# Kernel optimization log

Hardware: AMD Instinct MI355X
Metric: run time of the kernel (lower is better)

## Reference

```python
import jax, jax.numpy as jnp
import numpy as np

N = 100000   # nodes
E = 1600000  # edges
I_DIM = 512
H_DIM = 64   # hardcoded in GCNEncoder
Z_DIM = 64


def gcn_conv(x, W, b, src, dst, n):
    """GCNConv: D^{-1/2}(A+I)D^{-1/2} X W + b, edge weights = 1."""
    xw = x @ W  # [n, out]
    ones = jnp.ones(src.shape[0], dtype=xw.dtype)
    deg = jax.ops.segment_sum(ones, dst, num_segments=n) + 1.0  # +1 for self-loop
    dinv = jax.lax.rsqrt(deg)
    norm = dinv[src] * dinv[dst]  # [E]
    agg = jax.ops.segment_sum(xw[src] * norm[:, None], dst, num_segments=n)
    agg = agg + xw * (dinv * dinv)[:, None]  # self-loop term, norm = 1/deg
    return agg + b


def setup_inputs() -> dict:
    key = jax.random.key(0)
    ks = jax.random.split(key, 9)
    x = jax.random.normal(ks[0], (N, I_DIM), dtype=jnp.float32)
    edge_index = jax.random.randint(ks[1], (2, E), 0, N, dtype=jnp.int64)
    # glorot-ish init for weights
    W1 = jax.random.normal(ks[2], (I_DIM, H_DIM), jnp.float32) * (1.0 / np.sqrt(I_DIM))
    b1 = jnp.zeros((H_DIM,), jnp.float32)
    W_mu = jax.random.normal(ks[3], (H_DIM, Z_DIM), jnp.float32) * (1.0 / np.sqrt(H_DIM))
    b_mu = jnp.zeros((Z_DIM,), jnp.float32)
    W_var = jax.random.normal(ks[4], (H_DIM, Z_DIM), jnp.float32) * (1.0 / np.sqrt(H_DIM))
    b_var = jnp.zeros((Z_DIM,), jnp.float32)
    eps = jax.random.normal(ks[5], (N, Z_DIM), jnp.float32)  # reparameterization noise
    return {"x": x, "edge_index": edge_index, "W1": W1, "b1": b1,
            "W_mu": W_mu, "b_mu": b_mu, "W_var": W_var, "b_var": b_var,
            "eps": eps}


def reference(x, edge_index, W1, b1, W_mu, b_mu, W_var, b_var, eps):
    n = x.shape[0]
    src, dst = edge_index[0], edge_index[1]
    # encoder (eval mode: dropout is identity)
    h = jax.nn.relu(gcn_conv(x, W1, b1, src, dst, n))
    z_mean = gcn_conv(h, W_mu, b_mu, src, dst, n)
    z_var = jax.nn.softplus(gcn_conv(h, W_var, b_var, src, dst, n))
    # Normal(z_mean, z_var).rsample()
    z = z_mean + z_var * eps
    return z_mean, z_var, z
```

## Files before the change

kernel.cpp:

```cpp
#include <hip/hip_runtime.h>
#include <hip/hip_bf16.h>
#include <math.h>

#define IDIM 512
#define HDIM 64

typedef __attribute__((ext_vector_type(8))) short short8;
typedef __attribute__((ext_vector_type(4))) float f32x4;
typedef unsigned short u16;
typedef unsigned int u32;

__device__ __forceinline__ float bflo(u32 u) { return __uint_as_float(u << 16); }
__device__ __forceinline__ float bfhi(u32 u) { return __uint_as_float(u & 0xffff0000u); }


__global__ __launch_bounds__(256) void k_deg(const int* __restrict__ dst,
                                             int* __restrict__ deg, int E) {
    int e = blockIdx.x * blockDim.x + threadIdx.x;
    if (e < E) atomicAdd(&deg[dst[e]], 1);
}

__global__ __launch_bounds__(256) void k_blocksum(const int* __restrict__ deg,
                                                  int* __restrict__ bsum, int n) {
    __shared__ int sd[256];
    int b = blockIdx.x, tid = threadIdx.x;
    int base = b * 1024 + tid * 4;
    int s = 0;
#pragma unroll
    for (int k = 0; k < 4; k++) {
        int idx = base + k;
        if (idx < n) s += deg[idx];
    }
    sd[tid] = s;
    __syncthreads();
    for (int off = 128; off > 0; off >>= 1) {
        if (tid < off) sd[tid] += sd[tid + off];
        __syncthreads();
    }
    if (tid == 0) bsum[b] = sd[0];
}

__global__ __launch_bounds__(128) void k_scanbsum(const int* __restrict__ bsum,
                                                  int* __restrict__ boff, int B,
                                                  int* __restrict__ rowptr, int n, int E) {
    __shared__ int s[128];
    int t = threadIdx.x;
    int v = (t < B) ? bsum[t] : 0;
    s[t] = v;
    __syncthreads();
    for (int off = 1; off < 128; off <<= 1) {
        int u = (t >= off) ? s[t - off] : 0;
        __syncthreads();
        s[t] += u;
        __syncthreads();
    }
    if (t < B) boff[t] = s[t] - v;
    if (t == 0) rowptr[n] = E;
}

__global__ __launch_bounds__(256) void k_rowptr(const int* __restrict__ deg,
                                                const int* __restrict__ boff,
                                                int* __restrict__ rowptr,
                                                int* __restrict__ cursor,
                                                float* __restrict__ dinv, int n) {
    __shared__ int sd[256];
    int b = blockIdx.x, tid = threadIdx.x;
    int base = b * 1024 + tid * 4;
    int d[4];
    int tt = 0;
#pragma unroll
    for (int k = 0; k < 4; k++) {
        d[k] = (base + k < n) ? deg[base + k] : 0;
        tt += d[k];
    }
    sd[tid] = tt;
    __syncthreads();
    for (int off = 1; off < 256; off <<= 1) {
        int v = 0;
        if (tid >= off) v = sd[tid - off];
        __syncthreads();
        sd[tid] += v;
        __syncthreads();
    }
    int run = boff[b] + sd[tid] - tt;
#pragma unroll
    for (int k = 0; k < 4; k++) {
        if (base + k < n) {
            rowptr[base + k] = run;
            cursor[base + k] = run;
            dinv[base + k] = rsqrtf((float)d[k] + 1.0f);
            run += d[k];
        }
    }
}

__global__ __launch_bounds__(256) void k_build(const int* __restrict__ src,
                                               const int* __restrict__ dst,
                                               int* __restrict__ cursor,
                                               int* __restrict__ srcs, int E) {
    int e = blockIdx.x * blockDim.x + threadIdx.x;
    if (e >= E) return;
    int p = atomicAdd(&cursor[dst[e]], 1);
    srcs[p] = src[e];
}

__global__ __launch_bounds__(256) void k_prepB(const float* __restrict__ W1,
                                               short* __restrict__ Btg) {
    int id = blockIdx.x * 256 + threadIdx.x;
    if (id >= IDIM * HDIM) return;
    int k = id >> 6, nn = id & 63;
    __hip_bfloat16 b = __float2bfloat16(W1[id]);
    Btg[nn * IDIM + k] = *(short*)&b;
}

__global__ __launch_bounds__(256) void k_prepW2(const float* __restrict__ Wmu,
                                                const float* __restrict__ Wvar,
                                                short* __restrict__ Whi,
                                                short* __restrict__ Wlo) {
    int id = blockIdx.x * 256 + threadIdx.x;
    if (id >= 128 * 64) return;
    int c = id >> 6;
    int k = id & 63;
    float wv = (c < 64) ? Wmu[k * 64 + c] : Wvar[k * 64 + (c - 64)];
    __hip_bfloat16 h = __float2bfloat16(wv);
    float hf = __bfloat162float(h);
    __hip_bfloat16 l = __float2bfloat16(wv - hf);
    Whi[c * 64 + k] = *(short*)&h;
    Wlo[c * 64 + k] = *(short*)&l;
}

#define GM 128
#define KC 128
#define APAD 8
__global__ __launch_bounds__(256) void k_gemm1(const float* __restrict__ x,
                                               const short* __restrict__ Btg,
                                               const float* __restrict__ dinv,
                                               u16* __restrict__ g1, int n) {
    __shared__ short As[GM][KC + APAD];
    __shared__ short Bs[HDIM][KC + APAD];
    int tid = threadIdx.x;
    int row0 = blockIdx.x * GM;
    int w = tid >> 6, lane = tid & 63;
    int m = lane & 15, kb = lane >> 4;

    f32x4 acc[2][4];
#pragma unroll
    for (int rb = 0; rb < 2; rb++)
#pragma unroll
        for (int nt = 0; nt < 4; nt++) acc[rb][nt] = (f32x4){0.f, 0.f, 0.f, 0.f};

    for (int kc = 0; kc < IDIM; kc += KC) {
        __syncthreads();
#pragma unroll
        for (int i = 0; i < 16; i++) {
            int idx = tid + i * 256;
            int r = idx >> 5;
            int c4 = idx & 31;
            int grow = row0 + r;
            float4 v = make_float4(0.f, 0.f, 0.f, 0.f);
            if (grow < n) v = *(const float4*)&x[(size_t)grow * IDIM + kc + c4 * 4];
            __hip_bfloat162 h0 = __float22bfloat162_rn(make_float2(v.x, v.y));
            __hip_bfloat162 h1 = __float22bfloat162_rn(make_float2(v.z, v.w));
            int2 p;
            p.x = *(int*)&h0;
            p.y = *(int*)&h1;
            *(int2*)&As[r][c4 * 4] = p;
        }
#pragma unroll
        for (int i = 0; i < 4; i++) {
            int idx = tid + i * 256;
            int r = idx >> 4;
            int u8 = idx & 15;
            float4 v = *(const float4*)&Btg[(size_t)r * IDIM + kc + u8 * 8];
            *(float4*)&Bs[r][u8 * 8] = v;
        }
        __syncthreads();
#pragma unroll
        for (int ks = 0; ks < KC; ks += 32) {
            short8 a0 = *(const short8*)&As[w * 32 + m][ks + kb * 8];
            short8 a1 = *(const short8*)&As[w * 32 + 16 + m][ks + kb * 8];
            short8 b0 = *(const short8*)&Bs[m][ks + kb * 8];
            short8 b1 = *(const short8*)&Bs[16 + m][ks + kb * 8];
            short8 b2 = *(const short8*)&Bs[32 + m][ks + kb * 8];
            short8 b3 = *(const short8*)&Bs[48 + m][ks + kb * 8];
            acc[0][0] = __builtin_amdgcn_mfma_f32_16x16x32_bf16(a0, b0, acc[0][0], 0, 0, 0);
            acc[0][1] = __builtin_amdgcn_mfma_f32_16x16x32_bf16(a0, b1, acc[0][1], 0, 0, 0);
            acc[0][2] = __builtin_amdgcn_mfma_f32_16x16x32_bf16(a0, b2, acc[0][2], 0, 0, 0);
            acc[0][3] = __builtin_amdgcn_mfma_f32_16x16x32_bf16(a0, b3, acc[0][3], 0, 0, 0);
            acc[1][0] = __builtin_amdgcn_mfma_f32_16x16x32_bf16(a1, b0, acc[1][0], 0, 0, 0);
            acc[1][1] = __builtin_amdgcn_mfma_f32_16x16x32_bf16(a1, b1, acc[1][1], 0, 0, 0);
            acc[1][2] = __builtin_amdgcn_mfma_f32_16x16x32_bf16(a1, b2, acc[1][2], 0, 0, 0);
            acc[1][3] = __builtin_amdgcn_mfma_f32_16x16x32_bf16(a1, b3, acc[1][3], 0, 0, 0);
        }
    }
#pragma unroll
    for (int rb = 0; rb < 2; rb++) {
        int rbase = row0 + w * 32 + rb * 16 + kb * 4;
#pragma unroll
        for (int reg = 0; reg < 4; reg++) {
            int grow = rbase + reg;
            if (grow < n) {
                float dv = dinv[grow];
#pragma unroll
                for (int nt = 0; nt < 4; nt++) {
                    __hip_bfloat16 b = __float2bfloat16(acc[rb][nt][reg] * dv);
                    g1[(size_t)grow * HDIM + nt * 16 + m] = *(u16*)&b;
                }
            }
        }
    }
}

__global__ __launch_bounds__(256) void k_gather1(const int* __restrict__ rowptr,
                                                 const int* __restrict__ srcs,
                                                 const float* __restrict__ dinv,
                                                 const u16* __restrict__ g1,
                                                 const float* __restrict__ b1,
                                                 u16* __restrict__ g2, int n) {
    int tid = threadIdx.x;
    int r = tid >> 6, lane = tid & 63;
    int grp = lane >> 3, q = lane & 7;
    int i = blockIdx.x * 4 + r;
    if (i >= n) return;
    int beg = rowptr[i], end = rowptr[i + 1];
    float a[8];
#pragma unroll
    for (int k = 0; k < 8; k++) a[k] = 0.f;
    int j = beg + grp;
    for (; j + 8 < end; j += 16) {
        int s0 = srcs[j];
        int s1 = srcs[j + 8];
        uint4 u0 = *(const uint4*)&g1[(size_t)s0 * HDIM + q * 8];
        uint4 u1 = *(const uint4*)&g1[(size_t)s1 * HDIM + q * 8];
        a[0] += bflo(u0.x) + bflo(u1.x); a[1] += bfhi(u0.x) + bfhi(u1.x);
        a[2] += bflo(u0.y) + bflo(u1.y); a[3] += bfhi(u0.y) + bfhi(u1.y);
        a[4] += bflo(u0.z) + bflo(u1.z); a[5] += bfhi(u0.z) + bfhi(u1.z);
        a[6] += bflo(u0.w) + bflo(u1.w); a[7] += bfhi(u0.w) + bfhi(u1.w);
    }
    if (j < end) {
        int s0 = srcs[j];
        uint4 u0 = *(const uint4*)&g1[(size_t)s0 * HDIM + q * 8];
        a[0] += bflo(u0.x); a[1] += bfhi(u0.x);
        a[2] += bflo(u0.y); a[3] += bfhi(u0.y);
        a[4] += bflo(u0.z); a[5] += bfhi(u0.z);
        a[6] += bflo(u0.w); a[7] += bfhi(u0.w);
    }
#pragma unroll
    for (int k = 0; k < 8; k++) {
        a[k] += __shfl_xor(a[k], 8);
        a[k] += __shfl_xor(a[k], 16);
        a[k] += __shfl_xor(a[k], 32);
    }
    if (grp == 0) {
        uint4 us = *(const uint4*)&g1[(size_t)i * HDIM + q * 8];
        float s0 = bflo(us.x), s1 = bfhi(us.x), s2 = bflo(us.y), s3 = bfhi(us.y);
        float s4 = bflo(us.z), s5 = bfhi(us.z), s6 = bflo(us.w), s7 = bfhi(us.w);
        float4 bv0 = *(const float4*)&b1[q * 8];
        float4 bv1 = *(const float4*)&b1[q * 8 + 4];
        float di = dinv[i];
        float o0 = fmaxf(di * (a[0] + s0) + bv0.x, 0.f) * di;
        float o1 = fmaxf(di * (a[1] + s1) + bv0.y, 0.f) * di;
        float o2 = fmaxf(di * (a[2] + s2) + bv0.z, 0.f) * di;
        float o3 = fmaxf(di * (a[3] + s3) + bv0.w, 0.f) * di;
        float o4 = fmaxf(di * (a[4] + s4) + bv1.x, 0.f) * di;
        float o5 = fmaxf(di * (a[5] + s5) + bv1.y, 0.f) * di;
        float o6 = fmaxf(di * (a[6] + s6) + bv1.z, 0.f) * di;
        float o7 = fmaxf(di * (a[7] + s7) + bv1.w, 0.f) * di;
        __hip_bfloat162 p0 = __float22bfloat162_rn(make_float2(o0, o1));
        __hip_bfloat162 p1 = __float22bfloat162_rn(make_float2(o2, o3));
        __hip_bfloat162 p2 = __float22bfloat162_rn(make_float2(o4, o5));
        __hip_bfloat162 p3 = __float22bfloat162_rn(make_float2(o6, o7));
        uint4 w;
        w.x = *(u32*)&p0; w.y = *(u32*)&p1; w.z = *(u32*)&p2; w.w = *(u32*)&p3;
        *(uint4*)&g2[(size_t)i * HDIM + q * 8] = w;
    }
}

__global__ __launch_bounds__(256) void k_gather2(const int* __restrict__ rowptr,
                                                 const int* __restrict__ srcs,
                                                 const float* __restrict__ dinv,
                                                 const u16* __restrict__ g2,
                                                 float* __restrict__ hagg, int n) {
    int tid = threadIdx.x;
    int r = tid >> 6, lane = tid & 63;
    int grp = lane >> 3, q = lane & 7;
    int i = blockIdx.x * 4 + r;
    if (i >= n) return;
    int beg = rowptr[i], end = rowptr[i + 1];
    float a[8];
#pragma unroll
    for (int k = 0; k < 8; k++) a[k] = 0.f;
    int j = beg + grp;
    for (; j + 8 < end; j += 16) {
        int s0 = srcs[j];
        int s1 = srcs[j + 8];
        uint4 u0 = *(const uint4*)&g2[(size_t)s0 * HDIM + q * 8];
        uint4 u1 = *(const uint4*)&g2[(size_t)s1 * HDIM + q * 8];
        a[0] += bflo(u0.x) + bflo(u1.x); a[1] += bfhi(u0.x) + bfhi(u1.x);
        a[2] += bflo(u0.y) + bflo(u1.y); a[3] += bfhi(u0.y) + bfhi(u1.y);
        a[4] += bflo(u0.z) + bflo(u1.z); a[5] += bfhi(u0.z) + bfhi(u1.z);
        a[6] += bflo(u0.w) + bflo(u1.w); a[7] += bfhi(u0.w) + bfhi(u1.w);
    }
    if (j < end) {
        int s0 = srcs[j];
        uint4 u0 = *(const uint4*)&g2[(size_t)s0 * HDIM + q * 8];
        a[0] += bflo(u0.x); a[1] += bfhi(u0.x);
        a[2] += bflo(u0.y); a[3] += bfhi(u0.y);
        a[4] += bflo(u0.z); a[5] += bfhi(u0.z);
        a[6] += bflo(u0.w); a[7] += bfhi(u0.w);
    }
#pragma unroll
    for (int k = 0; k < 8; k++) {
        a[k] += __shfl_xor(a[k], 8);
        a[k] += __shfl_xor(a[k], 16);
        a[k] += __shfl_xor(a[k], 32);
    }
    if (grp == 0) {
        uint4 us = *(const uint4*)&g2[(size_t)i * HDIM + q * 8];
        float di = dinv[i];
        float4 o0, o1;
        o0.x = di * (a[0] + bflo(us.x));
        o0.y = di * (a[1] + bfhi(us.x));
        o0.z = di * (a[2] + bflo(us.y));
        o0.w = di * (a[3] + bfhi(us.y));
        o1.x = di * (a[4] + bflo(us.z));
        o1.y = di * (a[5] + bfhi(us.z));
        o1.z = di * (a[6] + bflo(us.w));
        o1.w = di * (a[7] + bfhi(us.w));
        *(float4*)&hagg[(size_t)i * HDIM + q * 8] = o0;
        *(float4*)&hagg[(size_t)i * HDIM + q * 8 + 4] = o1;
    }
}

__global__ __launch_bounds__(256) void k_gemm2(const float* __restrict__ hagg,
                                               const short* __restrict__ Whi,
                                               const short* __restrict__ Wlo,
                                               const float* __restrict__ bmu,
                                               const float* __restrict__ bvar,
                                               const float* __restrict__ eps,
                                               float* __restrict__ out, int n) {
    int tid = threadIdx.x;
    int w = tid >> 6, lane = tid & 63;
    int m = lane & 15, kb = lane >> 4;
    int row0 = blockIdx.x * 128 + w * 32;

    short8 ah[2][2], al[2][2];
#pragma unroll
    for (int rb = 0; rb < 2; rb++) {
#pragma unroll
        for (int ks = 0; ks < 2; ks++) {
            int grow = row0 + rb * 16 + m;
            float v[8];
            if (grow < n) {
                const float* base = &hagg[(size_t)grow * HDIM + ks * 32 + kb * 8];
                float4 v0 = *(const float4*)base;
                float4 v1 = *(const float4*)(base + 4);
                v[0] = v0.x; v[1] = v0.y; v[2] = v0.z; v[3] = v0.w;
                v[4] = v1.x; v[5] = v1.y; v[6] = v1.z; v[7] = v1.w;
            } else {
#pragma unroll
                for (int jj = 0; jj < 8; jj++) v[jj] = 0.f;
            }
#pragma unroll
            for (int jj = 0; jj < 8; jj++) {
                __hip_bfloat16 h = __float2bfloat16(v[jj]);
                float hf = __bfloat162float(h);
                __hip_bfloat16 l = __float2bfloat16(v[jj] - hf);
                ah[rb][ks][jj] = *(short*)&h;
                al[rb][ks][jj] = *(short*)&l;
            }
        }
    }

    f32x4 acc[2][8];
#pragma unroll
    for (int rb = 0; rb < 2; rb++)
#pragma unroll
        for (int nt = 0; nt < 8; nt++) acc[rb][nt] = (f32x4){0.f, 0.f, 0.f, 0.f};

#pragma unroll
    for (int nt = 0; nt < 8; nt++) {
#pragma unroll
        for (int ks = 0; ks < 2; ks++) {
            const short* bbase = &Whi[(size_t)(nt * 16 + m) * HDIM + ks * 32 + kb * 8];
            const short* lbase = &Wlo[(size_t)(nt * 16 + m) * HDIM + ks * 32 + kb * 8];
            short8 bh = *(const short8*)bbase;
            short8 bl = *(const short8*)lbase;
#pragma unroll
            for (int rb = 0; rb < 2; rb++) {
                acc[rb][nt] = __builtin_amdgcn_mfma_f32_16x16x32_bf16(ah[rb][ks], bh, acc[rb][nt], 0, 0, 0);
                acc[rb][nt] = __builtin_amdgcn_mfma_f32_16x16x32_bf16(al[rb][ks], bh, acc[rb][nt], 0, 0, 0);
                acc[rb][nt] = __builtin_amdgcn_mfma_f32_16x16x32_bf16(ah[rb][ks], bl, acc[rb][nt], 0, 0, 0);
            }
        }
    }

    size_t nh = (size_t)n * HDIM;
#pragma unroll
    for (int rb = 0; rb < 2; rb++) {
#pragma unroll
        for (int nt = 0; nt < 4; nt++) {
            int c = nt * 16 + m;
            float bm = bmu[c], bv = bvar[c];
#pragma unroll
            for (int reg = 0; reg < 4; reg++) {
                int grow = row0 + rb * 16 + kb * 4 + reg;
                if (grow < n) {
                    float mu = acc[rb][nt][reg] + bm;
                    float va = acc[rb][nt + 4][reg] + bv;
                    float zv = fmaxf(va, 0.f) + log1pf(expf(-fabsf(va)));
                    size_t o = (size_t)grow * HDIM + c;
                    float z = mu + zv * eps[o];
                    out[o] = mu;
                    out[nh + o] = zv;
                    out[2 * nh + o] = z;
                }
            }
        }
    }
}

extern "C" void kernel_launch(void* const* d_in, const int* in_sizes, int n_in,
                              void* d_out, int out_size, void* d_ws, size_t ws_size,
                              hipStream_t stream) {
    const float* x    = (const float*)d_in[0];
    const int*   ei   = (const int*)d_in[1];
    const float* W1   = (const float*)d_in[2];
    const float* b1   = (const float*)d_in[3];
    const float* Wmu  = (const float*)d_in[4];
    const float* bmu  = (const float*)d_in[5];
    const float* Wvar = (const float*)d_in[6];
    const float* bvar = (const float*)d_in[7];
    const float* eps  = (const float*)d_in[8];
    float* out = (float*)d_out;

    int n = in_sizes[0] / IDIM;
    int E = in_sizes[1] / 2;
    const int* src = ei;
    const int* dst = ei + E;

    char* p = (char*)d_ws;
    u16* bufB   = (u16*)p;               p += (size_t)n * HDIM * 2;
    float* hagg = (float*)p;             p += (size_t)n * HDIM * 4;
    u16* bufA   = (u16*)hagg;
    int* srcs   = (int*)p;               p += (size_t)E * 4;
    short* Btg  = (short*)p;             p += (size_t)IDIM * HDIM * 2;
    short* W2hi = (short*)p;             p += (size_t)128 * HDIM * 2;
    short* W2lo = (short*)p;             p += (size_t)128 * HDIM * 2;
    int* rowptr = (int*)p;               p += (size_t)(n + 1) * 4;
    int* cursor = (int*)p;               p += (size_t)n * 4;
    float* dinv = (float*)p;             p += (size_t)n * 4;
    int* bsum   = (int*)p;               p += 128 * 4;
    int* boff   = (int*)p;               p += 128 * 4;

    int B = (n + 1023) / 1024;

    hipMemsetAsync(cursor, 0, (size_t)n * sizeof(int), stream);
    k_deg<<<(E + 255) / 256, 256, 0, stream>>>(dst, cursor, E);
    k_blocksum<<<B, 256, 0, stream>>>(cursor, bsum, n);
    k_scanbsum<<<1, 128, 0, stream>>>(bsum, boff, B, rowptr, n, E);
    k_rowptr<<<B, 256, 0, stream>>>(cursor, boff, rowptr, cursor, dinv, n);
    k_build<<<(E + 255) / 256, 256, 0, stream>>>(src, dst, cursor, srcs, E);

    k_prepB<<<(IDIM * HDIM + 255) / 256, 256, 0, stream>>>(W1, Btg);
    k_prepW2<<<(128 * HDIM + 255) / 256, 256, 0, stream>>>(Wmu, Wvar, W2hi, W2lo);

    k_gemm1<<<(n + GM - 1) / GM, 256, 0, stream>>>(x, Btg, dinv, bufA, n);
    k_gather1<<<(n + 3) / 4, 256, 0, stream>>>(rowptr, srcs, dinv, bufA, b1, bufB, n);

    k_gather2<<<(n + 3) / 4, 256, 0, stream>>>(rowptr, srcs, dinv, bufB, hagg, n);
    k_gemm2<<<(n + 127) / 128, 256, 0, stream>>>(hagg, W2hi, W2lo, bmu, bvar, eps, out, n);
}
```

Measured before the change: 714.7 us.

## Build CSR via two-level bucket partition with shared-memory histograms; shrink GEMM1 K-chunk

Replaces the global-atomic degree count, three-kernel scan and atomic scatter CSR build with a coarse bucket scheme. Edges are bucketed by destination (512 nodes per bucket) using shared-memory histograms, then partitioned into a temporary int2 buffer. Each bucket is finalized in one block that computes local row pointers, dinv and srcs with shared-memory atomics. This removes scattered global atomics and random writes, at the cost of an extra pass over the edges and a temporary buffer that aliases hagg. GEMM1's K chunk is also halved, shrinking shared memory per block to allow higher occupancy.

```diff
diff --git a/kernel.cpp b/kernel.cpp
--- a/kernel.cpp
+++ b/kernel.cpp
@@ -4,6 +4,10 @@
 
 #define IDIM 512
 #define HDIM 64
+
+#define CB_SH 9
+#define CB_NODES 512
+#define PCHUNK 4096
 
 typedef __attribute__((ext_vector_type(8))) short short8;
 typedef __attribute__((ext_vector_type(4))) float f32x4;
@@ -14,94 +18,123 @@
 __device__ __forceinline__ float bfhi(u32 u) { return __uint_as_float(u & 0xffff0000u); }
 
 
-__global__ __launch_bounds__(256) void k_deg(const int* __restrict__ dst,
-                                             int* __restrict__ deg, int E) {
-    int e = blockIdx.x * blockDim.x + threadIdx.x;
-    if (e < E) atomicAdd(&deg[dst[e]], 1);
-}
-
-__global__ __launch_bounds__(256) void k_blocksum(const int* __restrict__ deg,
-                                                  int* __restrict__ bsum, int n) {
-    __shared__ int sd[256];
-    int b = blockIdx.x, tid = threadIdx.x;
-    int base = b * 1024 + tid * 4;
+__global__ __launch_bounds__(256) void k_chist(const int* __restrict__ dst,
+                                               int* __restrict__ gHist, int E, int NB) {
+    __shared__ int h[1024];
+    int tid = threadIdx.x;
+    for (int i = tid; i < NB; i += 256) h[i] = 0;
+    __syncthreads();
+    int stride = gridDim.x * 256;
+    for (int e = blockIdx.x * 256 + tid; e < E; e += stride)
+        atomicAdd(&h[dst[e] >> CB_SH], 1);
+    __syncthreads();
+    for (int i = tid; i < NB; i += 256)
+        if (h[i]) atomicAdd(&gHist[i], h[i]);
+}
+
+__global__ __launch_bounds__(256) void k_cscan(const int* __restrict__ gHist,
+                                               int* __restrict__ bucketBase,
+                                               int* __restrict__ gcur, int NB,
+                                               int* __restrict__ rowptr, int n, int E) {
+    __shared__ int ss[256];
+    int tid = threadIdx.x;
+    int v[4];
     int s = 0;
 #pragma unroll
     for (int k = 0; k < 4; k++) {
-        int idx = base + k;
-        if (idx < n) s += deg[idx];
-    }
-    sd[tid] = s;
-    __syncthreads();
-    for (int off = 128; off > 0; off >>= 1) {
-        if (tid < off) sd[tid] += sd[tid + off];
+        int i = tid * 4 + k;
+        v[k] = (i < NB) ? gHist[i] : 0;
+        s += v[k];
+    }
+    ss[tid] = s;
+    __syncthreads();
+    for (int o = 1; o < 256; o <<= 1) {
+        int u = (tid >= o) ? ss[tid - o] : 0;
         __syncthreads();
-    }
-    if (tid == 0) bsum[b] = sd[0];
-}
-
-__global__ __launch_bounds__(128) void k_scanbsum(const int* __restrict__ bsum,
-                                                  int* __restrict__ boff, int B,
-                                                  int* __restrict__ rowptr, int n, int E) {
-    __shared__ int s[128];
-    int t = threadIdx.x;
-    int v = (t < B) ? bsum[t] : 0;
-    s[t] = v;
-    __syncthreads();
-    for (int off = 1; off < 128; off <<= 1) {
-        int u = (t >= off) ? s[t - off] : 0;
+        ss[tid] += u;
         __syncthreads();
-        s[t] += u;
+    }
+    int ex = ss[tid] - s;
+#pragma unroll
+    for (int k = 0; k < 4; k++) {
+        int i = tid * 4 + k;
+        if (i < NB) { bucketBase[i] = ex; gcur[i] = ex; }
+        ex += v[k];
+    }
+    if (tid == 0) { bucketBase[NB] = E; rowptr[n] = E; }
+}
+
+__global__ __launch_bounds__(256) void k_partition(const int* __restrict__ src,
+                                                   const int* __restrict__ dst,
+                                                   int* __restrict__ gcur,
+                                                   int2* __restrict__ tmp, int E, int NB) {
+    __shared__ int h[1024];
+    __shared__ int base[1024];
+    int tid = threadIdx.x;
+    int e0 = blockIdx.x * PCHUNK;
+    int e1 = min(e0 + PCHUNK, E);
+    for (int i = tid; i < NB; i += 256) h[i] = 0;
+    __syncthreads();
+    for (int e = e0 + tid; e < e1; e += 256)
+        atomicAdd(&h[dst[e] >> CB_SH], 1);
+    __syncthreads();
+    for (int i = tid; i < NB; i += 256) {
+        int c = h[i];
+        base[i] = c ? atomicAdd(&gcur[i], c) : 0;
+        h[i] = 0;
+    }
+    __syncthreads();
+    for (int e = e0 + tid; e < e1; e += 256) {
+        int d = dst[e];
+        int b = d >> CB_SH;
+        int r = atomicAdd(&h[b], 1);
+        tmp[base[b] + r] = make_int2(src[e], d);
+    }
+}
+
+__global__ __launch_bounds__(256) void k_finalize(const int2* __restrict__ tmp,
+                                                  const int* __restrict__ bucketBase,
+                                                  int* __restrict__ rowptr,
+                                                  float* __restrict__ dinv,
+                                                  int* __restrict__ srcs, int n) {
+    __shared__ int hist[CB_NODES];
+    __shared__ int off[CB_NODES];
+    __shared__ int ss[256];
+    int b = blockIdx.x;
+    int tid = threadIdx.x;
+    int node0 = b << CB_SH;
+    int nloc = min(CB_NODES, n - node0);
+    int e0 = bucketBase[b], e1 = bucketBase[b + 1];
+    hist[tid] = 0;
+    hist[tid + 256] = 0;
+    __syncthreads();
+    for (int e = e0 + tid; e < e1; e += 256)
+        atomicAdd(&hist[tmp[e].y - node0], 1);
+    __syncthreads();
+    int v0 = hist[2 * tid], v1 = hist[2 * tid + 1];
+    int ps = v0 + v1;
+    ss[tid] = ps;
+    __syncthreads();
+    for (int o = 1; o < 256; o <<= 1) {
+        int u = (tid >= o) ? ss[tid - o] : 0;
         __syncthreads();
-    }
-    if (t < B) boff[t] = s[t] - v;
-    if (t == 0) rowptr[n] = E;
-}
-
-__global__ __launch_bounds__(256) void k_rowptr(const int* __restrict__ deg,
-                                                const int* __restrict__ boff,
-                                                int* __restrict__ rowptr,
-                                                int* __restrict__ cursor,
-                                                float* __restrict__ dinv, int n) {
-    __shared__ int sd[256];
-    int b = blockIdx.x, tid = threadIdx.x;
-    int base = b * 1024 + tid * 4;
-    int d[4];
-    int tt = 0;
-#pragma unroll
-    for (int k = 0; k < 4; k++) {
-        d[k] = (base + k < n) ? deg[base + k] : 0;
-        tt += d[k];
-    }
-    sd[tid] = tt;
-    __syncthreads();
-    for (int off = 1; off < 256; off <<= 1) {
-        int v = 0;
-        if (tid >= off) v = sd[tid - off];
+        ss[tid] += u;
         __syncthreads();
-        sd[tid] += v;
-        __syncthreads();
-    }
-    int run = boff[b] + sd[tid] - tt;
-#pragma unroll
-    for (int k = 0; k < 4; k++) {
-        if (base + k < n) {
-            rowptr[base + k] = run;
-            cursor[base + k] = run;
-            dinv[base + k] = rsqrtf((float)d[k] + 1.0f);
-            run += d[k];
-        }
-    }
-}
-
-__global__ __launch_bounds__(256) void k_build(const int* __restrict__ src,
-                                               const int* __restrict__ dst,
-                                               int* __restrict__ cursor,
-                                               int* __restrict__ srcs, int E) {
-    int e = blockIdx.x * blockDim.x + threadIdx.x;
-    if (e >= E) return;
-    int p = atomicAdd(&cursor[dst[e]], 1);
-    srcs[p] = src[e];
+    }
+    int ex = ss[tid] - ps;
+    off[2 * tid] = ex;
+    off[2 * tid + 1] = ex + v0;
+    __syncthreads();
+    for (int i = tid; i < nloc; i += 256) {
+        rowptr[node0 + i] = e0 + off[i];
+        dinv[node0 + i] = rsqrtf((float)hist[i] + 1.0f);
+    }
+    __syncthreads();
+    for (int e = e0 + tid; e < e1; e += 256) {
+        int2 p = tmp[e];
+        int r = atomicAdd(&off[p.y - node0], 1);
+        srcs[e0 + r] = p.x;
+    }
 }
 
 __global__ __launch_bounds__(256) void k_prepB(const float* __restrict__ W1,
@@ -130,7 +163,7 @@
 }
 
 #define GM 128
-#define KC 128
+#define KC 64
 #define APAD 8
 __global__ __launch_bounds__(256) void k_gemm1(const float* __restrict__ x,
                                                const short* __restrict__ Btg,
@@ -152,10 +185,10 @@
     for (int kc = 0; kc < IDIM; kc += KC) {
         __syncthreads();
 #pragma unroll
-        for (int i = 0; i < 16; i++) {
+        for (int i = 0; i < 8; i++) {
             int idx = tid + i * 256;
-            int r = idx >> 5;
-            int c4 = idx & 31;
+            int r = idx >> 4;
+            int c4 = idx & 15;
             int grow = row0 + r;
             float4 v = make_float4(0.f, 0.f, 0.f, 0.f);
             if (grow < n) v = *(const float4*)&x[(size_t)grow * IDIM + kc + c4 * 4];
@@ -167,10 +200,10 @@
             *(int2*)&As[r][c4 * 4] = p;
         }
 #pragma unroll
-        for (int i = 0; i < 4; i++) {
+        for (int i = 0; i < 2; i++) {
             int idx = tid + i * 256;
-            int r = idx >> 4;
-            int u8 = idx & 15;
+            int r = idx >> 3;
+            int u8 = idx & 7;
             float4 v = *(const float4*)&Btg[(size_t)r * IDIM + kc + u8 * 8];
             *(float4*)&Bs[r][u8 * 8] = v;
         }
@@ -439,28 +472,28 @@
     const int* src = ei;
     const int* dst = ei + E;
 
+    int NB = (n + CB_NODES - 1) >> CB_SH;
+
     char* p = (char*)d_ws;
     u16* bufB   = (u16*)p;               p += (size_t)n * HDIM * 2;
     float* hagg = (float*)p;             p += (size_t)n * HDIM * 4;
     u16* bufA   = (u16*)hagg;
+    int2* tmp   = (int2*)hagg;
     int* srcs   = (int*)p;               p += (size_t)E * 4;
     short* Btg  = (short*)p;             p += (size_t)IDIM * HDIM * 2;
     short* W2hi = (short*)p;             p += (size_t)128 * HDIM * 2;
     short* W2lo = (short*)p;             p += (size_t)128 * HDIM * 2;
     int* rowptr = (int*)p;               p += (size_t)(n + 1) * 4;
-    int* cursor = (int*)p;               p += (size_t)n * 4;
     float* dinv = (float*)p;             p += (size_t)n * 4;
-    int* bsum   = (int*)p;               p += 128 * 4;
-    int* boff   = (int*)p;               p += 128 * 4;
-
-    int B = (n + 1023) / 1024;
-
-    hipMemsetAsync(cursor, 0, (size_t)n * sizeof(int), stream);
-    k_deg<<<(E + 255) / 256, 256, 0, stream>>>(dst, cursor, E);
-    k_blocksum<<<B, 256, 0, stream>>>(cursor, bsum, n);
-    k_scanbsum<<<1, 128, 0, stream>>>(bsum, boff, B, rowptr, n, E);
-    k_rowptr<<<B, 256, 0, stream>>>(cursor, boff, rowptr, cursor, dinv, n);
-    k_build<<<(E + 255) / 256, 256, 0, stream>>>(src, dst, cursor, srcs, E);
+    int* gHist  = (int*)p;               p += 1024 * 4;
+    int* gcur   = (int*)p;               p += 1024 * 4;
+    int* bucketBase = (int*)p;           p += 1025 * 4;
+
+    hipMemsetAsync(gHist, 0, (size_t)NB * sizeof(int), stream);
+    k_chist<<<512, 256, 0, stream>>>(dst, gHist, E, NB);
+    k_cscan<<<1, 256, 0, stream>>>(gHist, bucketBase, gcur, NB, rowptr, n, E);
+    k_partition<<<(E + PCHUNK - 1) / PCHUNK, 256, 0, stream>>>(src, dst, gcur, tmp, E, NB);
+    k_finalize<<<NB, 256, 0, stream>>>(tmp, bucketBase, rowptr, dinv, srcs, n);
 
     k_prepB<<<(IDIM * HDIM + 255) / 256, 256, 0, stream>>>(W1, Btg);
     k_prepW2<<<(128 * HDIM + 255) / 256, 256, 0, stream>>>(Wmu, Wvar, W2hi, W2lo);
```

After: 574.0 us. 19.7% less time.
